# Performance work log

Hardware: AMD Instinct MI355X
Metric: run time of the kernel (lower is better)

## Reference

```python
import jax, jax.numpy as jnp
import numpy as np

N_USERS = 100000
N_ITEMS = 50000
N = N_USERS + N_ITEMS
NNZ = 10000000
D = 64
N_HOPS = 3
EDGE_DROP = 0.5
MESS_DROP = 0.1


def setup_inputs() -> dict:
    key = jax.random.key(0)
    ks = jax.random.split(key, 7)
    user_embed = jax.random.normal(ks[0], (N_USERS, D), dtype=jnp.float32) * 0.1
    item_embed = jax.random.normal(ks[1], (N_ITEMS, D), dtype=jnp.float32) * 0.1
    rows = jax.random.randint(ks[2], (NNZ,), 0, N, dtype=jnp.int32)
    cols = jax.random.randint(ks[3], (NNZ,), 0, N, dtype=jnp.int32)
    vals = jax.random.uniform(ks[4], (NNZ,), dtype=jnp.float32) * 0.01
    # dropout keep-masks (deterministic): keep prob = 1 - rate
    edge_mask = jax.random.uniform(ks[5], (N_HOPS, NNZ)) >= EDGE_DROP
    mess_mask = jax.random.uniform(ks[6], (N_HOPS, N, D)) >= MESS_DROP
    return {"user_embed": user_embed, "item_embed": item_embed,
            "rows": rows, "cols": cols, "vals": vals,
            "edge_mask": edge_mask, "mess_mask": mess_mask}


def _spmm(rows, cols, vals, x, n):
    # out[r] = sum_{e: rows[e]==r} vals[e] * x[cols[e]]
    msg = vals[:, None] * x[cols]  # [nnz, d]
    return jax.ops.segment_sum(msg, rows, num_segments=n)


def reference(user_embed, item_embed, rows, cols, vals, edge_mask, mess_mask):
    all_embed = jnp.concatenate([user_embed, item_embed], axis=0)  # [N, d]
    n = all_embed.shape[0]
    agg = all_embed
    embs = [all_embed]
    edge_scale = 1.0 / (1.0 - EDGE_DROP)
    mess_scale = 1.0 / (1.0 - MESS_DROP)
    for hop in range(N_HOPS):
        # edge dropout == zero dropped nnz values, scale survivors
        v = jnp.where(edge_mask[hop], vals, 0.0) * edge_scale
        agg = _spmm(rows, cols, v, agg, n)
        # message dropout
        agg = jnp.where(mess_mask[hop], agg, 0.0) * mess_scale
        embs.append(agg)
    embs = jnp.stack(embs, axis=1)  # [N, n_hops+1, d]
    return embs[:N_USERS], embs[N_USERS:]
```

## Files before the change

kernel.cpp:

```cpp
#include <hip/hip_runtime.h>

#define N_USERS 100000
#define N_ITEMS 50000
#define NTOT    150000
#define NNZ     10000000
#define D       64
#define NHOPS   3
#define EDGE_SCALE 2.0f
#define MESS_SCALE (1.0f/0.9f)

#define NREC_MAX (NNZ + 7 * NTOT)
#define NBKT ((NTOT + 255) / 256)
#define EPB  4096
#define NBLKA ((NNZ + EPB - 1) / EPB)

#define OFF_FLAG 0
#define OFF_CNT  256
#define OFF_RPTR (OFF_CNT  + 600064)
#define OFF_CUR  (OFF_RPTR + 600064)
#define OFF_BST  (OFF_CUR  + 600064)
#define OFF_BCUR (OFF_BST  + 4096)
#define OFF_REC  (OFF_BCUR + 4096)
#define OFF_STG  (OFF_REC  + (size_t)NREC_MAX * 8)
#define WS_BINNED ((size_t)OFF_STG + (size_t)NNZ * 8)
#define WS_OLD    ((size_t)OFF_REC + (size_t)NREC_MAX * 8)

__global__ void detect_mask_kernel(const unsigned int* __restrict__ em,
                                   int* __restrict__ flag) {
    __shared__ int s;
    if (threadIdx.x == 0) s = 0;
    __syncthreads();
    for (int i = threadIdx.x; i < 1024; i += blockDim.x) {
        unsigned int w = em[i];
        if (w != 0u && w != 1u && w != 0x3f800000u) s = 1;
    }
    __syncthreads();
    if (threadIdx.x == 0) *flag = s;
}

__global__ void init_kernel(const float4* __restrict__ user,
                            const float4* __restrict__ item,
                            float4* __restrict__ out) {
    int i = blockIdx.x * blockDim.x + threadIdx.x;
    if (i >= NTOT * 16) return;
    int n = i >> 4, q = i & 15;
    float4 v = (n < N_USERS) ? user[(size_t)n * 16 + q]
                             : item[(size_t)(n - N_USERS) * 16 + q];
    out[(size_t)n * 64 + q] = v;
}

__global__ void hist_kernel(const int* __restrict__ rows, int* __restrict__ cnt) {
    int e = blockIdx.x * blockDim.x + threadIdx.x;
    if (e < NNZ) atomicAdd(&cnt[rows[e]], 1);
}

#define PAD8(c) (((c) + 7) & ~7)

__global__ void scan1_kernel(const int* __restrict__ cnt, int* __restrict__ part) {
    __shared__ int s[256];
    int b = blockIdx.x, t = threadIdx.x;
    int base = b * 1024 + t * 4, sum = 0;
    #pragma unroll
    for (int k = 0; k < 4; ++k) { int i = base + k; if (i < NTOT) sum += PAD8(cnt[i]); }
    s[t] = sum; __syncthreads();
    for (int off = 128; off > 0; off >>= 1) {
        if (t < off) s[t] += s[t + off];
        __syncthreads();
    }
    if (t == 0) part[b] = s[0];
}

__global__ void scan2_kernel(int* __restrict__ part, int npart) {
    __shared__ int s[256];
    int t = threadIdx.x;
    int my = (t < npart) ? part[t] : 0;
    s[t] = my; __syncthreads();
    for (int off = 1; off < 256; off <<= 1) {
        int v = (t >= off) ? s[t - off] : 0;
        __syncthreads();
        s[t] += v;
        __syncthreads();
    }
    if (t < npart) part[t] = s[t] - my;
}

__global__ void scan3_kernel(const int* __restrict__ cnt, const int* __restrict__ part,
                             int* __restrict__ rptr, int* __restrict__ cur) {
    __shared__ int s[256];
    int b = blockIdx.x, t = threadIdx.x;
    int base = b * 1024 + t * 4;
    int v[4], sum = 0;
    #pragma unroll
    for (int k = 0; k < 4; ++k) {
        int i = base + k;
        v[k] = (i < NTOT) ? PAD8(cnt[i]) : 0;
        sum += v[k];
    }
    int my = sum;
    s[t] = sum; __syncthreads();
    for (int off = 1; off < 256; off <<= 1) {
        int x = (t >= off) ? s[t - off] : 0;
        __syncthreads();
        s[t] += x;
        __syncthreads();
    }
    int run = s[t] - my + part[b];
    #pragma unroll
    for (int k = 0; k < 4; ++k) {
        int i = base + k;
        if (i < NTOT) { rptr[i] = run; cur[i] = run; }
        run += v[k];
    }
}

__global__ void fixtot_kernel(const int* __restrict__ cnt, int* __restrict__ rptr) {
    __shared__ int s[256];
    int t = threadIdx.x, sum = 0;
    for (int i = t; i < NTOT; i += 256) sum += PAD8(cnt[i]);
    s[t] = sum; __syncthreads();
    for (int off = 128; off > 0; off >>= 1) {
        if (t < off) s[t] += s[t + off];
        __syncthreads();
    }
    if (t == 0) rptr[NTOT] = s[0];
}

__global__ void pad_kernel(const int* __restrict__ rptr, const int* __restrict__ cnt,
                           uint2* __restrict__ rec) {
    int r = blockIdx.x * blockDim.x + threadIdx.x;
    if (r >= NTOT) return;
    int b = rptr[r] + cnt[r], e = rptr[r + 1];
    for (int j = b; j < e; ++j) rec[j] = make_uint2(0u, 0u);
}

__global__ __launch_bounds__(256) void binA_kernel(
        const int* __restrict__ rows, const int* __restrict__ cols,
        const float* __restrict__ vals,
        const void* __restrict__ emask, const int* __restrict__ flag,
        int* __restrict__ bcur, uint2* __restrict__ staged) {
    __shared__ int h[NBKT];
    int t = threadIdx.x;
    long long base = (long long)blockIdx.x * EPB;
    for (int b = t; b < NBKT; b += 256) h[b] = 0;
    __syncthreads();
    unsigned int rw[16];
    unsigned short rnk[16];
    #pragma unroll
    for (int k = 0; k < 16; ++k) {
        long long e = base + (long long)k * 256 + t;
        rw[k] = 0xFFFFFFFFu; rnk[k] = 0;
        if (e < NNZ) {
            unsigned int r = (unsigned int)rows[e];
            rw[k] = r;
            rnk[k] = (unsigned short)atomicAdd(&h[r >> 8], 1);
        }
    }
    __syncthreads();
    for (int b = t; b < NBKT; b += 256) {
        int c = h[b];
        h[b] = c ? atomicAdd(&bcur[b], c) : 0;
    }
    __syncthreads();
    bool bytes = (*flag != 0);
    #pragma unroll
    for (int k = 0; k < 16; ++k) {
        long long e = base + (long long)k * 256 + t;
        if (e < NNZ) {
            unsigned int r = rw[k];
            unsigned int p = (unsigned int)cols[e] & 0x3FFFFu;
            unsigned int m;
            if (bytes) {
                const unsigned char* em = (const unsigned char*)emask;
                m = (em[e] ? 1u : 0u)
                  | ((em[(size_t)NNZ + e] ? 1u : 0u) << 1)
                  | ((em[2 * (size_t)NNZ + e] ? 1u : 0u) << 2);
            } else {
                const unsigned int* em = (const unsigned int*)emask;
                m = (em[e] ? 1u : 0u)
                  | ((em[(size_t)NNZ + e] ? 1u : 0u) << 1)
                  | ((em[2 * (size_t)NNZ + e] ? 1u : 0u) << 2);
            }
            p |= m << 18;
            p |= (r & 255u) << 21;
            float v = vals[e] * EDGE_SCALE;
            int pos = h[r >> 8] + (int)rnk[k];
            staged[pos] = make_uint2(p, __float_as_uint(v));
        }
    }
}

__global__ void bsum_kernel(const int* __restrict__ cnt, int* __restrict__ bsum) {
    __shared__ int s[256];
    int b = blockIdx.x, t = threadIdx.x;
    int i = b * 256 + t;
    s[t] = (i < NTOT) ? cnt[i] : 0;
    __syncthreads();
    for (int off = 128; off > 0; off >>= 1) {
        if (t < off) s[t] += s[t + off];
        __syncthreads();
    }
    if (t == 0) bsum[b] = s[0];
}

__global__ void bscan_kernel(int* __restrict__ bst, int* __restrict__ bcur) {
    __shared__ int s[NBKT];
    int t = threadIdx.x;
    for (int b = t; b < NBKT; b += 256) s[b] = bcur[b];
    __syncthreads();
    if (t == 0) {
        int run = 0;
        for (int b = 0; b < NBKT; ++b) { int c = s[b]; s[b] = run; run += c; }
        bst[NBKT] = run;
    }
    __syncthreads();
    for (int b = t; b < NBKT; b += 256) { bst[b] = s[b]; bcur[b] = s[b]; }
}

__global__ __launch_bounds__(256) void binB_kernel(
        const int* __restrict__ rptr, const int* __restrict__ bst,
        const uint2* __restrict__ staged, uint2* __restrict__ rec) {
    __shared__ int lc[256];
    int b = blockIdx.x, t = threadIdx.x;
    int gr = b * 256 + t;
    lc[t] = (gr < NTOT) ? rptr[gr] : 0;
    __syncthreads();
    int s0 = bst[b], s1 = bst[b + 1];
    for (int i = s0 + t; i < s1; i += 256) {
        uint2 e = staged[i];
        int r8 = (int)((e.x >> 21) & 255u);
        int pos = atomicAdd(&lc[r8], 1);
        unsigned int cw = (e.x & 0x3FFFFu) | (((e.x >> 18) & 7u) << 24);
        rec[pos] = make_uint2(cw, e.y);
    }
}

__global__ void build_kernel(const int* __restrict__ rows, const int* __restrict__ cols,
                             const float* __restrict__ vals,
                             const void* __restrict__ emask, const int* __restrict__ flag,
                             int* __restrict__ cur, uint2* __restrict__ rec) {
    int e = blockIdx.x * blockDim.x + threadIdx.x;
    if (e >= NNZ) return;
    int pos = atomicAdd(&cur[rows[e]], 1);
    float v = vals[e] * EDGE_SCALE;
    unsigned int cw = (unsigned int)cols[e];
    if (*flag) {
        const unsigned char* em = (const unsigned char*)emask;
        cw |= (em[e] ? 1u : 0u) << 24;
        cw |= (em[(size_t)NNZ + e] ? 1u : 0u) << 25;
        cw |= (em[(size_t)2 * NNZ + e] ? 1u : 0u) << 26;
    } else {
        const unsigned int* em = (const unsigned int*)emask;
        cw |= (em[e] ? 1u : 0u) << 24;
        cw |= (em[(size_t)NNZ + e] ? 1u : 0u) << 25;
        cw |= (em[(size_t)2 * NNZ + e] ? 1u : 0u) << 26;
    }
    rec[pos] = make_uint2(cw, __float_as_uint(v));
}

template <int HOP>
__global__ __launch_bounds__(256) void hop_kernel(
        const uint2* __restrict__ rec,
        const int*   __restrict__ rptr,
        const void*  __restrict__ mmask,
        const int*   __restrict__ flag,
        float*       __restrict__ out) {
    int r    = blockIdx.x * 4 + (threadIdx.x >> 6);
    int lane = threadIdx.x & 63;
    if (r >= NTOT) return;
    int beg = __builtin_amdgcn_readfirstlane(rptr[r]);
    int end = __builtin_amdgcn_readfirstlane(rptr[r + 1]);

    const unsigned long long* __restrict__ rp = (const unsigned long long*)rec;
    const float* __restrict__ src = out + HOP * 64 + lane;
    float a0 = 0.0f, a1 = 0.0f, a2 = 0.0f, a3 = 0.0f;

    for (int i = beg; i < end; i += 8) {
        #pragma unroll
        for (int k = 0; k < 8; ++k) {
            unsigned long long rr = __builtin_nontemporal_load(&rp[i + k]);
            unsigned int ex = (unsigned int)rr;
            unsigned int keep = (ex >> (24 + HOP)) & 1u;
            unsigned int roff = keep ? (ex & 0x3FFFFu) * 256u : 0u;
            float v = keep ? __uint_as_float((unsigned int)(rr >> 32)) : 0.0f;
            float x = src[roff];
            if (k % 4 == 0) a0 += v * x;
            else if (k % 4 == 1) a1 += v * x;
            else if (k % 4 == 2) a2 += v * x;
            else a3 += v * x;
        }
    }
    float acc = (a0 + a1) + (a2 + a3);

    size_t mi = (size_t)HOP * NTOT * D + (size_t)r * D + lane;
    bool keep;
    if (*flag) keep = ((const unsigned char*)mmask)[mi] != 0;
    else       keep = ((const unsigned int*)mmask)[mi]  != 0;
    out[(size_t)r * 256 + (HOP + 1) * 64 + lane] = keep ? acc * MESS_SCALE : 0.0f;
}

__global__ __launch_bounds__(256) void scatter_fb_kernel(
        const int* __restrict__ rows, const int* __restrict__ cols,
        const float* __restrict__ vals, const void* __restrict__ emask,
        const int* __restrict__ flag, float* __restrict__ out, int hop) {
    int wid  = blockIdx.x * 4 + (threadIdx.x >> 6);
    int lane = threadIdx.x & 63;
    if (wid >= NNZ) return;
    size_t mi = (size_t)hop * NNZ + wid;
    bool keep;
    if (*flag) keep = ((const unsigned char*)emask)[mi] != 0;
    else       keep = ((const unsigned int*)emask)[mi]  != 0;
    if (!keep) return;
    float v = vals[wid] * EDGE_SCALE;
    float x = out[(size_t)cols[wid] * 256 + (size_t)hop * 64 + lane];
    atomicAdd(&out[(size_t)rows[wid] * 256 + (size_t)(hop + 1) * 64 + lane], v * x);
}

__global__ void mess_fb_kernel(const void* __restrict__ mmask, const int* __restrict__ flag,
                               float* __restrict__ out, int hop) {
    int i = blockIdx.x * blockDim.x + threadIdx.x;
    if (i >= NTOT * D) return;
    int n = i >> 6, d = i & 63;
    size_t mi = (size_t)hop * NTOT * D + i;
    bool keep;
    if (*flag) keep = ((const unsigned char*)mmask)[mi] != 0;
    else       keep = ((const unsigned int*)mmask)[mi]  != 0;
    size_t oi = (size_t)n * 256 + (size_t)(hop + 1) * 64 + d;
    out[oi] = keep ? out[oi] * MESS_SCALE : 0.0f;
}

extern "C" void kernel_launch(void* const* d_in, const int* in_sizes, int n_in,
                              void* d_out, int out_size, void* d_ws, size_t ws_size,
                              hipStream_t stream) {
    const float* user  = (const float*)d_in[0];
    const float* item  = (const float*)d_in[1];
    const int*   rows  = (const int*)d_in[2];
    const int*   cols  = (const int*)d_in[3];
    const float* vals  = (const float*)d_in[4];
    const void*  emask = d_in[5];
    const void*  mmask = d_in[6];
    float* out = (float*)d_out;

    char* ws = (char*)d_ws;
    int*   flag = (int*)(ws + OFF_FLAG);
    int*   cnt  = (int*)(ws + OFF_CNT);
    int*   rptr = (int*)(ws + OFF_RPTR);
    int*   cur  = (int*)(ws + OFF_CUR);
    int*   bst  = (int*)(ws + OFF_BST);
    int*   bcur = (int*)(ws + OFF_BCUR);
    uint2* rec  = (uint2*)(ws + OFF_REC);
    uint2* stg  = (uint2*)(ws + OFF_STG);
    int*   part = (int*)(ws + OFF_REC);

    detect_mask_kernel<<<1, 256, 0, stream>>>((const unsigned int*)emask, flag);

    if (ws_size >= WS_OLD) {
        hipMemsetAsync(cnt, 0, (size_t)NTOT * sizeof(int), stream);
        hist_kernel<<<(NNZ + 255) / 256, 256, 0, stream>>>(rows, cnt);
        const int NB = (NTOT + 1023) / 1024;
        scan1_kernel<<<NB, 256, 0, stream>>>(cnt, part);
        scan2_kernel<<<1, 256, 0, stream>>>(part, NB);
        scan3_kernel<<<NB, 256, 0, stream>>>(cnt, part, rptr, cur);
        fixtot_kernel<<<1, 256, 0, stream>>>(cnt, rptr);
        pad_kernel<<<(NTOT + 255) / 256, 256, 0, stream>>>(rptr, cnt, rec);

        if (ws_size >= WS_BINNED) {
            bsum_kernel<<<NBKT, 256, 0, stream>>>(cnt, bcur);
            bscan_kernel<<<1, 256, 0, stream>>>(bst, bcur);
            binA_kernel<<<NBLKA, 256, 0, stream>>>(
                rows, cols, vals, emask, flag, bcur, stg);
            binB_kernel<<<NBKT, 256, 0, stream>>>(rptr, bst, stg, rec);
        } else {
            build_kernel<<<(NNZ + 255) / 256, 256, 0, stream>>>(
                rows, cols, vals, emask, flag, cur, rec);
        }

        init_kernel<<<(NTOT * 16 + 255) / 256, 256, 0, stream>>>(
            (const float4*)user, (const float4*)item, (float4*)out);
        const int HB = (NTOT + 3) / 4;
        hop_kernel<0><<<HB, 256, 0, stream>>>(rec, rptr, mmask, flag, out);
        hop_kernel<1><<<HB, 256, 0, stream>>>(rec, rptr, mmask, flag, out);
        hop_kernel<2><<<HB, 256, 0, stream>>>(rec, rptr, mmask, flag, out);
    } else {
        hipMemsetAsync(d_out, 0, (size_t)out_size * sizeof(float), stream);
        init_kernel<<<(NTOT * 16 + 255) / 256, 256, 0, stream>>>(
            (const float4*)user, (const float4*)item, (float4*)out);
        for (int hop = 0; hop < NHOPS; ++hop) {
            scatter_fb_kernel<<<(NNZ + 3) / 4, 256, 0, stream>>>(
                rows, cols, vals, emask, flag, out, hop);
            mess_fb_kernel<<<(NTOT * D + 255) / 256, 256, 0, stream>>>(
                mmask, flag, out, hop);
        }
    }
}
```

Before: 1.820 ms.

## Replace global per-row atomic histogram with bucket counts and post-binning row counts

The old path built per-row counts with 10M global atomics on a 150K-entry array before binning. The new path counts only per-256-row buckets using shared-memory histograms in a persistent grid, bins edges into buckets, and then derives per-row counts from the bucketed staging buffer with shared atomics. The row-pointer scan, padding and final binB placement follow after that. This is meant to remove contended global atomics and one full random-access pass, at the cost of an extra read of the staged buffer.

```diff
diff --git a/kernel.cpp b/kernel.cpp
--- a/kernel.cpp
+++ b/kernel.cpp
@@ -13,6 +13,7 @@
 #define NBKT ((NTOT + 255) / 256)
 #define EPB  4096
 #define NBLKA ((NNZ + EPB - 1) / EPB)
+#define NBLK_BC 592
 
 #define OFF_FLAG 0
 #define OFF_CNT  256
@@ -49,88 +50,34 @@
     out[(size_t)n * 64 + q] = v;
 }
 
-__global__ void hist_kernel(const int* __restrict__ rows, int* __restrict__ cnt) {
-    int e = blockIdx.x * blockDim.x + threadIdx.x;
-    if (e < NNZ) atomicAdd(&cnt[rows[e]], 1);
-}
-
-#define PAD8(c) (((c) + 7) & ~7)
-
-__global__ void scan1_kernel(const int* __restrict__ cnt, int* __restrict__ part) {
-    __shared__ int s[256];
-    int b = blockIdx.x, t = threadIdx.x;
-    int base = b * 1024 + t * 4, sum = 0;
-    #pragma unroll
-    for (int k = 0; k < 4; ++k) { int i = base + k; if (i < NTOT) sum += PAD8(cnt[i]); }
-    s[t] = sum; __syncthreads();
-    for (int off = 128; off > 0; off >>= 1) {
-        if (t < off) s[t] += s[t + off];
-        __syncthreads();
-    }
-    if (t == 0) part[b] = s[0];
-}
-
-__global__ void scan2_kernel(int* __restrict__ part, int npart) {
-    __shared__ int s[256];
+__global__ __launch_bounds__(256) void bktcnt_kernel(const int* __restrict__ rows,
+                                                     int* __restrict__ bsum) {
+    __shared__ int h[NBKT];
     int t = threadIdx.x;
-    int my = (t < npart) ? part[t] : 0;
-    s[t] = my; __syncthreads();
-    for (int off = 1; off < 256; off <<= 1) {
-        int v = (t >= off) ? s[t - off] : 0;
-        __syncthreads();
-        s[t] += v;
-        __syncthreads();
-    }
-    if (t < npart) part[t] = s[t] - my;
-}
-
-__global__ void scan3_kernel(const int* __restrict__ cnt, const int* __restrict__ part,
-                             int* __restrict__ rptr, int* __restrict__ cur) {
-    __shared__ int s[256];
-    int b = blockIdx.x, t = threadIdx.x;
-    int base = b * 1024 + t * 4;
-    int v[4], sum = 0;
-    #pragma unroll
-    for (int k = 0; k < 4; ++k) {
-        int i = base + k;
-        v[k] = (i < NTOT) ? PAD8(cnt[i]) : 0;
-        sum += v[k];
-    }
-    int my = sum;
-    s[t] = sum; __syncthreads();
-    for (int off = 1; off < 256; off <<= 1) {
-        int x = (t >= off) ? s[t - off] : 0;
-        __syncthreads();
-        s[t] += x;
-        __syncthreads();
-    }
-    int run = s[t] - my + part[b];
-    #pragma unroll
-    for (int k = 0; k < 4; ++k) {
-        int i = base + k;
-        if (i < NTOT) { rptr[i] = run; cur[i] = run; }
-        run += v[k];
-    }
-}
-
-__global__ void fixtot_kernel(const int* __restrict__ cnt, int* __restrict__ rptr) {
-    __shared__ int s[256];
-    int t = threadIdx.x, sum = 0;
-    for (int i = t; i < NTOT; i += 256) sum += PAD8(cnt[i]);
-    s[t] = sum; __syncthreads();
-    for (int off = 128; off > 0; off >>= 1) {
-        if (t < off) s[t] += s[t + off];
-        __syncthreads();
-    }
-    if (t == 0) rptr[NTOT] = s[0];
-}
-
-__global__ void pad_kernel(const int* __restrict__ rptr, const int* __restrict__ cnt,
-                           uint2* __restrict__ rec) {
-    int r = blockIdx.x * blockDim.x + threadIdx.x;
-    if (r >= NTOT) return;
-    int b = rptr[r] + cnt[r], e = rptr[r + 1];
-    for (int j = b; j < e; ++j) rec[j] = make_uint2(0u, 0u);
+    for (int b = t; b < NBKT; b += 256) h[b] = 0;
+    __syncthreads();
+    for (long long e = (long long)blockIdx.x * 256 + t; e < NNZ;
+         e += (long long)NBLK_BC * 256)
+        atomicAdd(&h[((unsigned int)rows[e]) >> 8], 1);
+    __syncthreads();
+    for (int b = t; b < NBKT; b += 256) {
+        int c = h[b];
+        if (c) atomicAdd(&bsum[b], c);
+    }
+}
+
+__global__ void bscan_kernel(int* __restrict__ bst, int* __restrict__ bcur) {
+    __shared__ int s[NBKT];
+    int t = threadIdx.x;
+    for (int b = t; b < NBKT; b += 256) s[b] = bcur[b];
+    __syncthreads();
+    if (t == 0) {
+        int run = 0;
+        for (int b = 0; b < NBKT; ++b) { int c = s[b]; s[b] = run; run += c; }
+        bst[NBKT] = run;
+    }
+    __syncthreads();
+    for (int b = t; b < NBKT; b += 256) { bst[b] = s[b]; bcur[b] = s[b]; }
 }
 
 __global__ __launch_bounds__(256) void binA_kernel(
@@ -189,31 +136,103 @@
     }
 }
 
-__global__ void bsum_kernel(const int* __restrict__ cnt, int* __restrict__ bsum) {
+__global__ __launch_bounds__(256) void bcnt_kernel(const int* __restrict__ bst,
+                                                   const uint2* __restrict__ staged,
+                                                   int* __restrict__ cnt) {
+    __shared__ int h[256];
+    int b = blockIdx.x, t = threadIdx.x;
+    h[t] = 0;
+    __syncthreads();
+    int s0 = bst[b], s1 = bst[b + 1];
+    for (int i = s0 + t; i < s1; i += 256)
+        atomicAdd(&h[(staged[i].x >> 21) & 255u], 1);
+    __syncthreads();
+    int gr = b * 256 + t;
+    if (gr < NTOT) cnt[gr] = h[t];
+}
+
+__global__ void hist_kernel(const int* __restrict__ rows, int* __restrict__ cnt) {
+    int e = blockIdx.x * blockDim.x + threadIdx.x;
+    if (e < NNZ) atomicAdd(&cnt[rows[e]], 1);
+}
+
+#define PAD8(c) (((c) + 7) & ~7)
+
+__global__ void scan1_kernel(const int* __restrict__ cnt, int* __restrict__ part) {
     __shared__ int s[256];
     int b = blockIdx.x, t = threadIdx.x;
-    int i = b * 256 + t;
-    s[t] = (i < NTOT) ? cnt[i] : 0;
-    __syncthreads();
+    int base = b * 1024 + t * 4, sum = 0;
+    #pragma unroll
+    for (int k = 0; k < 4; ++k) { int i = base + k; if (i < NTOT) sum += PAD8(cnt[i]); }
+    s[t] = sum; __syncthreads();
     for (int off = 128; off > 0; off >>= 1) {
         if (t < off) s[t] += s[t + off];
         __syncthreads();
     }
-    if (t == 0) bsum[b] = s[0];
-}
-
-__global__ void bscan_kernel(int* __restrict__ bst, int* __restrict__ bcur) {
-    __shared__ int s[NBKT];
+    if (t == 0) part[b] = s[0];
+}
+
+__global__ void scan2_kernel(int* __restrict__ part, int npart) {
+    __shared__ int s[256];
     int t = threadIdx.x;
-    for (int b = t; b < NBKT; b += 256) s[b] = bcur[b];
-    __syncthreads();
-    if (t == 0) {
-        int run = 0;
-        for (int b = 0; b < NBKT; ++b) { int c = s[b]; s[b] = run; run += c; }
-        bst[NBKT] = run;
-    }
-    __syncthreads();
-    for (int b = t; b < NBKT; b += 256) { bst[b] = s[b]; bcur[b] = s[b]; }
+    int my = (t < npart) ? part[t] : 0;
+    s[t] = my; __syncthreads();
+    for (int off = 1; off < 256; off <<= 1) {
+        int v = (t >= off) ? s[t - off] : 0;
+        __syncthreads();
+        s[t] += v;
+        __syncthreads();
+    }
+    if (t < npart) part[t] = s[t] - my;
+}
+
+__global__ void scan3_kernel(const int* __restrict__ cnt, const int* __restrict__ part,
+                             int* __restrict__ rptr, int* __restrict__ cur) {
+    __shared__ int s[256];
+    int b = blockIdx.x, t = threadIdx.x;
+    int base = b * 1024 + t * 4;
+    int v[4], sum = 0;
+    #pragma unroll
+    for (int k = 0; k < 4; ++k) {
+        int i = base + k;
+        v[k] = (i < NTOT) ? PAD8(cnt[i]) : 0;
+        sum += v[k];
+    }
+    int my = sum;
+    s[t] = sum; __syncthreads();
+    for (int off = 1; off < 256; off <<= 1) {
+        int x = (t >= off) ? s[t - off] : 0;
+        __syncthreads();
+        s[t] += x;
+        __syncthreads();
+    }
+    int run = s[t] - my + part[b];
+    #pragma unroll
+    for (int k = 0; k < 4; ++k) {
+        int i = base + k;
+        if (i < NTOT) { rptr[i] = run; cur[i] = run; }
+        run += v[k];
+    }
+}
+
+__global__ void fixtot_kernel(const int* __restrict__ cnt, int* __restrict__ rptr) {
+    __shared__ int s[256];
+    int t = threadIdx.x, sum = 0;
+    for (int i = t; i < NTOT; i += 256) sum += PAD8(cnt[i]);
+    s[t] = sum; __syncthreads();
+    for (int off = 128; off > 0; off >>= 1) {
+        if (t < off) s[t] += s[t + off];
+        __syncthreads();
+    }
+    if (t == 0) rptr[NTOT] = s[0];
+}
+
+__global__ void pad_kernel(const int* __restrict__ rptr, const int* __restrict__ cnt,
+                           uint2* __restrict__ rec) {
+    int r = blockIdx.x * blockDim.x + threadIdx.x;
+    if (r >= NTOT) return;
+    int b = rptr[r] + cnt[r], e = rptr[r + 1];
+    for (int j = b; j < e; ++j) rec[j] = make_uint2(0u, 0u);
 }
 
 __global__ __launch_bounds__(256) void binB_kernel(
@@ -353,27 +372,37 @@
 
     detect_mask_kernel<<<1, 256, 0, stream>>>((const unsigned int*)emask, flag);
 
-    if (ws_size >= WS_OLD) {
-        hipMemsetAsync(cnt, 0, (size_t)NTOT * sizeof(int), stream);
-        hist_kernel<<<(NNZ + 255) / 256, 256, 0, stream>>>(rows, cnt);
-        const int NB = (NTOT + 1023) / 1024;
+    const int NB = (NTOT + 1023) / 1024;
+
+    if (ws_size >= WS_BINNED) {
+        hipMemsetAsync(bcur, 0, 4096, stream);
+        bktcnt_kernel<<<NBLK_BC, 256, 0, stream>>>(rows, bcur);
+        bscan_kernel<<<1, 256, 0, stream>>>(bst, bcur);
+        binA_kernel<<<NBLKA, 256, 0, stream>>>(
+            rows, cols, vals, emask, flag, bcur, stg);
+        bcnt_kernel<<<NBKT, 256, 0, stream>>>(bst, stg, cnt);
         scan1_kernel<<<NB, 256, 0, stream>>>(cnt, part);
         scan2_kernel<<<1, 256, 0, stream>>>(part, NB);
         scan3_kernel<<<NB, 256, 0, stream>>>(cnt, part, rptr, cur);
         fixtot_kernel<<<1, 256, 0, stream>>>(cnt, rptr);
         pad_kernel<<<(NTOT + 255) / 256, 256, 0, stream>>>(rptr, cnt, rec);
-
-        if (ws_size >= WS_BINNED) {
-            bsum_kernel<<<NBKT, 256, 0, stream>>>(cnt, bcur);
-            bscan_kernel<<<1, 256, 0, stream>>>(bst, bcur);
-            binA_kernel<<<NBLKA, 256, 0, stream>>>(
-                rows, cols, vals, emask, flag, bcur, stg);
-            binB_kernel<<<NBKT, 256, 0, stream>>>(rptr, bst, stg, rec);
-        } else {
-            build_kernel<<<(NNZ + 255) / 256, 256, 0, stream>>>(
-                rows, cols, vals, emask, flag, cur, rec);
-        }
-
+        binB_kernel<<<NBKT, 256, 0, stream>>>(rptr, bst, stg, rec);
+        init_kernel<<<(NTOT * 16 + 255) / 256, 256, 0, stream>>>(
+            (const float4*)user, (const float4*)item, (float4*)out);
+        const int HB = (NTOT + 3) / 4;
+        hop_kernel<0><<<HB, 256, 0, stream>>>(rec, rptr, mmask, flag, out);
+        hop_kernel<1><<<HB, 256, 0, stream>>>(rec, rptr, mmask, flag, out);
+        hop_kernel<2><<<HB, 256, 0, stream>>>(rec, rptr, mmask, flag, out);
+    } else if (ws_size >= WS_OLD) {
+        hipMemsetAsync(cnt, 0, (size_t)NTOT * sizeof(int), stream);
+        hist_kernel<<<(NNZ + 255) / 256, 256, 0, stream>>>(rows, cnt);
+        scan1_kernel<<<NB, 256, 0, stream>>>(cnt, part);
+        scan2_kernel<<<1, 256, 0, stream>>>(part, NB);
+        scan3_kernel<<<NB, 256, 0, stream>>>(cnt, part, rptr, cur);
+        fixtot_kernel<<<1, 256, 0, stream>>>(cnt, rptr);
+        pad_kernel<<<(NTOT + 255) / 256, 256, 0, stream>>>(rptr, cnt, rec);
+        build_kernel<<<(NNZ + 255) / 256, 256, 0, stream>>>(
+            rows, cols, vals, emask, flag, cur, rec);
         init_kernel<<<(NTOT * 16 + 255) / 256, 256, 0, stream>>>(
             (const float4*)user, (const float4*)item, (float4*)out);
         const int HB = (NTOT + 3) / 4;
```

After: 1.490 ms. 18.1% less time.
